# Kernel optimization log

Hardware: AMD Instinct MI355X
Metric: run time of the kernel (lower is better)

The kernel has to match this reference:

```python
import math
import jax, jax.numpy as jnp
import numpy as np

WS = 16        # window size (square)
SHIFT = 8      # window_size // 2 (window_shift=True)
NUM_HEADS = 6

def _rel_coords_table(ws):
    # Swin-V2 log-spaced continuous relative coords, shape (1, 2ws-1, 2ws-1, 2)
    r = np.arange(-(ws - 1), ws, dtype=np.float32)
    t = np.stack(np.meshgrid(r, r, indexing='ij'), axis=-1)[None]
    t = t / (ws - 1) * 8.0
    t = np.sign(t) * np.log2(np.abs(t) + 1.0) / np.log2(8.0)
    return t.astype(np.float32)

def _rel_pos_index(ws):
    ch, cw = np.meshgrid(np.arange(ws), np.arange(ws), indexing='ij')
    coords = np.stack([ch.ravel(), cw.ravel()])          # (2, N)
    rel = coords[:, :, None] - coords[:, None, :]        # (2, N, N)
    rel = rel.transpose(1, 2, 0).astype(np.int64)
    rel[..., 0] += ws - 1
    rel[..., 1] += ws - 1
    rel[..., 0] *= 2 * ws - 1
    return rel.sum(-1).astype(np.int32)                  # (N, N), values in [0, (2ws-1)^2)

def _shift_mask(H, W, ws, shift):
    img = np.zeros((H, W), dtype=np.float32)
    cnt = 0
    for hs in (slice(0, -ws), slice(-ws, -shift), slice(-shift, None)):
        for wsl in (slice(0, -ws), slice(-ws, -shift), slice(-shift, None)):
            img[hs, wsl] = cnt; cnt += 1
    win = img.reshape(H // ws, ws, W // ws, ws).transpose(0, 2, 1, 3).reshape(-1, ws * ws)
    diff = win[:, None, :] - win[:, :, None]
    return np.where(diff != 0, -100.0, 0.0).astype(np.float32)  # (nW, N, N)

def setup_inputs():
    key = jax.random.key(0)
    ks = jax.random.split(key, 4)
    B, H, W = 16, 64, 64
    C = 3 * NUM_HEADS * 32  # 576 (qkv channels)
    qkv = jax.random.normal(ks[0], (B, H * W, C), dtype=jnp.float32)
    table = jnp.asarray(_rel_coords_table(WS))
    index = jnp.asarray(_rel_pos_index(WS))
    mask = jnp.asarray(_shift_mask(H, W, WS, SHIFT))
    logit_scale = jnp.log(10.0 * jnp.ones((NUM_HEADS, 1, 1), dtype=jnp.float32))
    w1 = jax.random.normal(ks[1], (512, 2), dtype=jnp.float32) * 0.02
    b1 = jnp.zeros((512,), dtype=jnp.float32)
    w2 = jax.random.normal(ks[2], (NUM_HEADS, 512), dtype=jnp.float32) * 0.02
    return {"qkv": qkv, "table": table, "mask": mask, "logit_scale": logit_scale,
            "w1": w1, "b1": b1, "w2": w2, "index": index, "H": H, "W": W}

def reference(qkv, table, mask, logit_scale, w1, b1, w2, index, H, W):
    B, L, C = qkv.shape
    dim = C // 3
    hd = dim // NUM_HEADS
    x = qkv.reshape(B, H, W, C)
    x = jnp.roll(x, (-SHIFT, -SHIFT), axis=(1, 2))
    nWh, nWw = H // WS, W // WS
    # window partition -> (B_, N, C)
    x = x.reshape(B, nWh, WS, nWw, WS, C).transpose(0, 1, 3, 2, 4, 5).reshape(-1, WS * WS, C)
    B_, N, _ = x.shape
    qkv_ = x.reshape(B_, N, 3, NUM_HEADS, hd).transpose(2, 0, 3, 1, 4)
    q, k, v = qkv_[0], qkv_[1], qkv_[2]  # (B_, H, N, hd)
    # cosine attention
    qn = q / jnp.maximum(jnp.linalg.norm(q, axis=-1, keepdims=True), 1e-12)
    kn = k / jnp.maximum(jnp.linalg.norm(k, axis=-1, keepdims=True), 1e-12)
    attn = jnp.einsum('bhnd,bhmd->bhnm', qn, kn)
    scale = jnp.exp(jnp.minimum(logit_scale, math.log(1.0 / 0.01)))  # (H,1,1)
    attn = attn * scale[None]
    # CPB MLP bias: Linear(2,512)+ReLU -> Linear(512,H,no bias)
    hidden = jax.nn.relu(table @ w1.T + b1)          # (1, 2ws-1, 2ws-1, 512)
    bias_table = (hidden @ w2.T).reshape(-1, NUM_HEADS)
    bias = bias_table[index.reshape(-1)].reshape(N, N, NUM_HEADS).transpose(2, 0, 1)
    attn = attn + 16.0 * jax.nn.sigmoid(bias)[None]
    # shifted-window mask
    nWm = mask.shape[0]
    attn = attn.reshape(B_ // nWm, nWm, NUM_HEADS, N, N) + mask[None, :, None]
    attn = attn.reshape(B_, NUM_HEADS, N, N)
    attn = jax.nn.softmax(attn, axis=-1)
    out = jnp.einsum('bhnm,bhmd->bhnd', attn, v)
    out = out.transpose(0, 2, 1, 3).reshape(B_, N, dim)
    # window reverse + unshift
    out = out.reshape(B, nWh, nWw, WS, WS, dim).transpose(0, 1, 3, 2, 4, 5).reshape(B, H, W, dim)
    out = jnp.roll(out, (SHIFT, SHIFT), axis=(1, 2))
    return out.reshape(B, L, dim)
```

## Files before the change

kernel.cpp:

```cpp
#include <hip/hip_runtime.h>
#include <cstdint>

#define NH 6
#define HD 32
#define NTOK 256
#define CIN 576
#define DIMO 192
#define LOG2E 1.44269504f
#define SHIFT2 37.6f
#define MNEG (-144.269504f)

typedef short short8 __attribute__((ext_vector_type(8)));
typedef float f32x4 __attribute__((ext_vector_type(4)));

__device__ __forceinline__ int grp6(int x) { return (x < 48) ? 0 : ((x < 56) ? 1 : 2); }

__device__ __forceinline__ unsigned short f2bf(float f) {
    unsigned int u = __float_as_uint(f);
    u += 0x7fffu + ((u >> 16) & 1u);
    return (unsigned short)(u >> 16);
}
__device__ __forceinline__ float bf2f(unsigned short s) {
    return __uint_as_float(((unsigned)s) << 16);
}

__global__ void cpb_kernel(const float* __restrict__ table,
                           const float* __restrict__ w1,
                           const float* __restrict__ b1,
                           const float* __restrict__ w2,
                           float* __restrict__ bv) {
    __shared__ float hid[512];
    int p = blockIdx.x;
    float t0 = table[2 * p], t1 = table[2 * p + 1];
    int t = threadIdx.x;
    for (int j = t; j < 512; j += 256) {
        float hv = fmaf(t0, w1[2 * j], fmaf(t1, w1[2 * j + 1], b1[j]));
        hid[j] = fmaxf(hv, 0.f);
    }
    __syncthreads();
    if (t < 192) {
        int h = t >> 5, l = t & 31;
        const float* w2h = w2 + h * 512;
        float acc = 0.f;
        for (int j = l; j < 512; j += 32) acc = fmaf(hid[j], w2h[j], acc);
        acc += __shfl_xor(acc, 1, 32);
        acc += __shfl_xor(acc, 2, 32);
        acc += __shfl_xor(acc, 4, 32);
        acc += __shfl_xor(acc, 8, 32);
        acc += __shfl_xor(acc, 16, 32);
        if (l == 0) bv[h * 961 + p] = (16.f / (1.f + __expf(-acc))) * LOG2E;
    }
}

__global__ __launch_bounds__(512, 4) void attn_kernel(
    const float* __restrict__ qkv,
    const float* __restrict__ logit_scale,
    const float* __restrict__ bv,
    float* __restrict__ out)
{
    __shared__ __align__(16) short Qb[NTOK * HD];
    __shared__ __align__(16) short Kb[NTOK * HD];
    __shared__ __align__(16) short Vt[HD * 264];
    __shared__ __align__(16) short P[8 * 32 * 32];
    __shared__ float Bv[961];

    const int t = threadIdx.x;
    const int h = blockIdx.x % NH;
    const int win = blockIdx.x / NH;
    const int b = win >> 4, wl = win & 15, wh = wl >> 2, ww = wl & 3;

    const float scale2 = __expf(fminf(logit_scale[h], 4.6051702f)) * LOG2E;

    for (int p = t; p < 961; p += 512) Bv[p] = bv[h * 961 + p];

    {
        int n = (t < 256) ? t : (t - 256);
        int i = n >> 4, j = n & 15;
        int rr = wh * 16 + i, cc = ww * 16 + j;
        int r = (rr + 8) & 63, c = (cc + 8) & 63;
        const float* base = qkv + ((long)(b * 4096 + r * 64 + c)) * CIN + h * HD;
        if (t < 256) {
            float qv[32], kv[32];
            const float4* qp = (const float4*)base;
            const float4* kp = (const float4*)(base + DIMO);
#pragma unroll
            for (int w = 0; w < 8; ++w) {
                float4 x = qp[w];
                qv[4 * w + 0] = x.x; qv[4 * w + 1] = x.y; qv[4 * w + 2] = x.z; qv[4 * w + 3] = x.w;
            }
#pragma unroll
            for (int w = 0; w < 8; ++w) {
                float4 x = kp[w];
                kv[4 * w + 0] = x.x; kv[4 * w + 1] = x.y; kv[4 * w + 2] = x.z; kv[4 * w + 3] = x.w;
            }
            float sq = 0.f, sk = 0.f;
#pragma unroll
            for (int d = 0; d < 32; ++d) { sq = fmaf(qv[d], qv[d], sq); sk = fmaf(kv[d], kv[d], sk); }
            float qs = scale2 / fmaxf(sqrtf(sq), 1e-12f);
            float ks = 1.f / fmaxf(sqrtf(sk), 1e-12f);
#pragma unroll
            for (int w = 0; w < 4; ++w) {
                short8 qc, kc;
#pragma unroll
                for (int e = 0; e < 8; ++e) {
                    qc[e] = (short)f2bf(qv[8 * w + e] * qs);
                    kc[e] = (short)f2bf(kv[8 * w + e] * ks);
                }
                *(short8*)&Qb[n * 32 + 8 * w] = qc;
                *(short8*)&Kb[n * 32 + 8 * w] = kc;
            }
        } else {
            float vv[32];
            const float4* vp = (const float4*)(base + 2 * DIMO);
#pragma unroll
            for (int w = 0; w < 8; ++w) {
                float4 x = vp[w];
                vv[4 * w + 0] = x.x; vv[4 * w + 1] = x.y; vv[4 * w + 2] = x.z; vv[4 * w + 3] = x.w;
            }
#pragma unroll
            for (int d = 0; d < 32; ++d) Vt[d * 264 + n] = (short)f2bf(vv[d]);
        }
    }
    __syncthreads();

    const int wv = t >> 6, lane = t & 63, quad = lane >> 4, l15 = lane & 15;
    short* Pw = P + wv * 1024;

    int trg[2];
    short8 aQ[2];
#pragma unroll
    for (int tl = 0; tl < 2; ++tl) {
        trg[tl] = wv * 2 + tl;
        aQ[tl] = *(const short8*)&Qb[(trg[tl] * 16 + l15) * 32 + quad * 8];
    }
    int gqi[2];
#pragma unroll
    for (int tl = 0; tl < 2; ++tl) gqi[tl] = grp6(wh * 16 + trg[tl]);
    int gqj[4];
#pragma unroll
    for (int reg = 0; reg < 4; ++reg) gqj[reg] = grp6(ww * 16 + quad * 4 + reg);
    const int gmj = grp6(ww * 16 + l15);

    f32x4 O[2][2];
    float lp[2][4];
#pragma unroll
    for (int tl = 0; tl < 2; ++tl)
#pragma unroll
        for (int dtk = 0; dtk < 2; ++dtk) O[tl][dtk] = (f32x4){0.f, 0.f, 0.f, 0.f};
#pragma unroll
    for (int tl = 0; tl < 2; ++tl)
#pragma unroll
        for (int reg = 0; reg < 4; ++reg) lp[tl][reg] = 0.f;

    const f32x4 Zero = (f32x4){0.f, 0.f, 0.f, 0.f};

    for (int c = 0; c < 8; ++c) {
        short8 bK[2];
        int gmi[2], ctg[2];
#pragma unroll
        for (int ct = 0; ct < 2; ++ct) {
            ctg[ct] = c * 2 + ct;
            bK[ct] = *(const short8*)&Kb[(ctg[ct] * 16 + l15) * 32 + quad * 8];
            gmi[ct] = grp6(wh * 16 + ctg[ct]);
        }
        f32x4 S[2][2];
#pragma unroll
        for (int tl = 0; tl < 2; ++tl)
#pragma unroll
            for (int ct = 0; ct < 2; ++ct)
                S[tl][ct] = __builtin_amdgcn_mfma_f32_16x16x32_bf16(aQ[tl], bK[ct], Zero, 0, 0, 0);

#pragma unroll
        for (int tl = 0; tl < 2; ++tl) {
#pragma unroll
            for (int ct = 0; ct < 2; ++ct) {
                int rbase = (trg[tl] - ctg[ct] + 15) * 31 + 15 - l15;
                bool mi = (gqi[tl] == gmi[ct]);
#pragma unroll
                for (int reg = 0; reg < 4; ++reg) {
                    float bias = Bv[rbase + quad * 4 + reg];
                    float mterm = (mi && (gqj[reg] == gmj)) ? 0.f : MNEG;
                    float arg = S[tl][ct][reg] + bias + mterm - SHIFT2;
                    float e = __builtin_amdgcn_exp2f(arg);
                    unsigned short pb = f2bf(e);
                    lp[tl][reg] += bf2f(pb);
                    Pw[(tl * 16 + quad * 4 + reg) * 32 + ct * 16 + l15] = (short)pb;
                }
            }
        }

        short8 aP[2], bV[2];
#pragma unroll
        for (int tl = 0; tl < 2; ++tl)
            aP[tl] = *(const short8*)&Pw[(tl * 16 + l15) * 32 + quad * 8];
#pragma unroll
        for (int dtk = 0; dtk < 2; ++dtk)
            bV[dtk] = *(const short8*)&Vt[(dtk * 16 + l15) * 264 + c * 32 + quad * 8];
#pragma unroll
        for (int tl = 0; tl < 2; ++tl)
#pragma unroll
            for (int dtk = 0; dtk < 2; ++dtk)
                O[tl][dtk] = __builtin_amdgcn_mfma_f32_16x16x32_bf16(aP[tl], bV[dtk], O[tl][dtk], 0, 0, 0);
    }

#pragma unroll
    for (int tl = 0; tl < 2; ++tl)
#pragma unroll
        for (int reg = 0; reg < 4; ++reg) {
            float s = lp[tl][reg];
            s += __shfl_xor(s, 1, 16);
            s += __shfl_xor(s, 2, 16);
            s += __shfl_xor(s, 4, 16);
            s += __shfl_xor(s, 8, 16);
            lp[tl][reg] = 1.f / s;
        }

    const long pixb = (long)b * 4096;
#pragma unroll
    for (int tl = 0; tl < 2; ++tl) {
        int r = (wh * 16 + trg[tl] + 8) & 63;
#pragma unroll
        for (int reg = 0; reg < 4; ++reg) {
            int cpix = (ww * 16 + quad * 4 + reg + 8) & 63;
            float* op = out + (pixb + r * 64 + cpix) * DIMO + h * HD + l15;
            float inv = lp[tl][reg];
            op[0]  = O[tl][0][reg] * inv;
            op[16] = O[tl][1][reg] * inv;
        }
    }
}

extern "C" void kernel_launch(void* const* d_in, const int* in_sizes, int n_in,
                              void* d_out, int out_size, void* d_ws, size_t ws_size,
                              hipStream_t stream) {
    const float* qkv         = (const float*)d_in[0];
    const float* table       = (const float*)d_in[1];
    const float* logit_scale = (const float*)d_in[3];
    const float* w1          = (const float*)d_in[4];
    const float* b1          = (const float*)d_in[5];
    const float* w2          = (const float*)d_in[6];
    float* out = (float*)d_out;
    float* bv  = (float*)d_ws;

    cpb_kernel<<<961, 256, 0, stream>>>(table, w1, b1, w2, bv);
    attn_kernel<<<256 * NH, 512, 0, stream>>>(qkv, logit_scale, bv, out);
}
```

Baseline: 264.7 us.

## Keep softmax probabilities in registers via transposed S and permlane swap

Computes S transposed (K as the A operand, Q as the B operand) so that each lane holds probabilities for one query. The probabilities are then packed to bf16 with v_cvt_pk_bf16_f32 and rearranged with v_permlane32_swap into the MFMA A-operand layout, removing the per-wave P shared-memory round trip. The change also XOR-swizzles the Q/K LDS layout to cut bank conflicts, and permutes and pairs the V-transpose stores as 32-bit writes. It folds the SHIFT2 constant into the bias table and sums probabilities in fp32 instead of their rounded bf16 values, which slightly changes the softmax normalization numerics.

```diff
diff --git a/kernel.cpp b/kernel.cpp
--- a/kernel.cpp
+++ b/kernel.cpp
@@ -12,6 +12,7 @@
 
 typedef short short8 __attribute__((ext_vector_type(8)));
 typedef float f32x4 __attribute__((ext_vector_type(4)));
+typedef int   int4v __attribute__((ext_vector_type(4)));
 
 __device__ __forceinline__ int grp6(int x) { return (x < 48) ? 0 : ((x < 56) ? 1 : 2); }
 
@@ -20,8 +21,9 @@
     u += 0x7fffu + ((u >> 16) & 1u);
     return (unsigned short)(u >> 16);
 }
-__device__ __forceinline__ float bf2f(unsigned short s) {
-    return __uint_as_float(((unsigned)s) << 16);
+
+__device__ __forceinline__ int qk_off(int tile, int row, int quad) {
+    return tile * 512 + row * 32 + ((quad ^ ((row >> 1) & 3)) << 3);
 }
 
 __global__ void cpb_kernel(const float* __restrict__ table,
@@ -48,7 +50,7 @@
         acc += __shfl_xor(acc, 4, 32);
         acc += __shfl_xor(acc, 8, 32);
         acc += __shfl_xor(acc, 16, 32);
-        if (l == 0) bv[h * 961 + p] = (16.f / (1.f + __expf(-acc))) * LOG2E;
+        if (l == 0) bv[h * 961 + p] = (16.f / (1.f + __expf(-acc))) * LOG2E - SHIFT2;
     }
 }
 
@@ -61,7 +63,6 @@
     __shared__ __align__(16) short Qb[NTOK * HD];
     __shared__ __align__(16) short Kb[NTOK * HD];
     __shared__ __align__(16) short Vt[HD * 264];
-    __shared__ __align__(16) short P[8 * 32 * 32];
     __shared__ float Bv[961];
 
     const int t = threadIdx.x;
@@ -74,12 +75,12 @@
     for (int p = t; p < 961; p += 512) Bv[p] = bv[h * 961 + p];
 
     {
-        int n = (t < 256) ? t : (t - 256);
-        int i = n >> 4, j = n & 15;
-        int rr = wh * 16 + i, cc = ww * 16 + j;
-        int r = (rr + 8) & 63, c = (cc + 8) & 63;
-        const float* base = qkv + ((long)(b * 4096 + r * 64 + c)) * CIN + h * HD;
         if (t < 256) {
+            int n = t;
+            int i = n >> 4, j = n & 15;
+            int rr = wh * 16 + i, cc = ww * 16 + j;
+            int r = (rr + 8) & 63, c0 = (cc + 8) & 63;
+            const float* base = qkv + ((long)(b * 4096 + r * 64 + c0)) * CIN + h * HD;
             float qv[32], kv[32];
             const float4* qp = (const float4*)base;
             const float4* kp = (const float4*)(base + DIMO);
@@ -106,126 +107,133 @@
                     qc[e] = (short)f2bf(qv[8 * w + e] * qs);
                     kc[e] = (short)f2bf(kv[8 * w + e] * ks);
                 }
-                *(short8*)&Qb[n * 32 + 8 * w] = qc;
-                *(short8*)&Kb[n * 32 + 8 * w] = kc;
+                int off = qk_off(i, j, w);
+                *(short8*)&Qb[off] = qc;
+                *(short8*)&Kb[off] = kc;
             }
         } else {
-            float vv[32];
-            const float4* vp = (const float4*)(base + 2 * DIMO);
-#pragma unroll
-            for (int w = 0; w < 8; ++w) {
-                float4 x = vp[w];
-                vv[4 * w + 0] = x.x; vv[4 * w + 1] = x.y; vv[4 * w + 2] = x.z; vv[4 * w + 3] = x.w;
-            }
-#pragma unroll
-            for (int d = 0; d < 32; ++d) Vt[d * 264 + n] = (short)f2bf(vv[d]);
+            int n2 = t - 256;
+            int m = n2 & 127, dh = n2 >> 7;
+            int i = m >> 3;
+            int ja = (2 * m) & 15;
+            int r  = (wh * 16 + i + 8) & 63;
+            int ca = (ww * 16 + ja + 8) & 63;
+            int cb = (ww * 16 + ja + 1 + 8) & 63;
+            const float* ba = qkv + ((long)(b * 4096 + r * 64 + ca)) * CIN + h * HD + 2 * DIMO + dh * 16;
+            const float* bb = qkv + ((long)(b * 4096 + r * 64 + cb)) * CIN + h * HD + 2 * DIMO + dh * 16;
+            float va[16], vb[16];
+            const float4* pa4 = (const float4*)ba;
+            const float4* pb4 = (const float4*)bb;
+#pragma unroll
+            for (int w = 0; w < 4; ++w) {
+                float4 A = pa4[w], B = pb4[w];
+                va[4 * w + 0] = A.x; va[4 * w + 1] = A.y; va[4 * w + 2] = A.z; va[4 * w + 3] = A.w;
+                vb[4 * w + 0] = B.x; vb[4 * w + 1] = B.y; vb[4 * w + 2] = B.z; vb[4 * w + 3] = B.w;
+            }
+            int u = m & 15;
+            int jp = ((u & 1) << 3) | ((u & 2) << 1) | ((u & 4) >> 1) | ((u & 8) >> 3);
+            int colb = (m >> 4) * 32 + 2 * jp;
+#pragma unroll
+            for (int di = 0; di < 16; ++di) {
+                unsigned pa_ = f2bf(va[di]);
+                unsigned pb_ = f2bf(vb[di]);
+                *(unsigned*)&Vt[(dh * 16 + di) * 264 + colb] = pa_ | (pb_ << 16);
+            }
         }
     }
     __syncthreads();
 
     const int wv = t >> 6, lane = t & 63, quad = lane >> 4, l15 = lane & 15;
-    short* Pw = P + wv * 1024;
-
-    int trg[2];
-    short8 aQ[2];
-#pragma unroll
-    for (int tl = 0; tl < 2; ++tl) {
-        trg[tl] = wv * 2 + tl;
-        aQ[tl] = *(const short8*)&Qb[(trg[tl] * 16 + l15) * 32 + quad * 8];
-    }
-    int gqi[2];
-#pragma unroll
-    for (int tl = 0; tl < 2; ++tl) gqi[tl] = grp6(wh * 16 + trg[tl]);
-    int gqj[4];
-#pragma unroll
-    for (int reg = 0; reg < 4; ++reg) gqj[reg] = grp6(ww * 16 + quad * 4 + reg);
-    const int gmj = grp6(ww * 16 + l15);
+
+    int trg[2] = {wv * 2, wv * 2 + 1};
+    short8 bQ[2];
+#pragma unroll
+    for (int tl = 0; tl < 2; ++tl)
+        bQ[tl] = *(const short8*)&Qb[qk_off(trg[tl], l15, quad)];
+
+    int gqr[2];
+#pragma unroll
+    for (int tl = 0; tl < 2; ++tl) gqr[tl] = grp6(wh * 16 + trg[tl]);
+    const int gcl = grp6(ww * 16 + l15);
+    float cm[4];
+#pragma unroll
+    for (int reg = 0; reg < 4; ++reg)
+        cm[reg] = (gcl == grp6(ww * 16 + quad * 4 + reg)) ? 0.f : MNEG;
 
     f32x4 O[2][2];
-    float lp[2][4];
+    float lp[2] = {0.f, 0.f};
 #pragma unroll
     for (int tl = 0; tl < 2; ++tl)
 #pragma unroll
         for (int dtk = 0; dtk < 2; ++dtk) O[tl][dtk] = (f32x4){0.f, 0.f, 0.f, 0.f};
-#pragma unroll
-    for (int tl = 0; tl < 2; ++tl)
-#pragma unroll
-        for (int reg = 0; reg < 4; ++reg) lp[tl][reg] = 0.f;
 
     const f32x4 Zero = (f32x4){0.f, 0.f, 0.f, 0.f};
 
     for (int c = 0; c < 8; ++c) {
-        short8 bK[2];
-        int gmi[2], ctg[2];
-#pragma unroll
-        for (int ct = 0; ct < 2; ++ct) {
-            ctg[ct] = c * 2 + ct;
-            bK[ct] = *(const short8*)&Kb[(ctg[ct] * 16 + l15) * 32 + quad * 8];
-            gmi[ct] = grp6(wh * 16 + ctg[ct]);
-        }
-        f32x4 S[2][2];
-#pragma unroll
-        for (int tl = 0; tl < 2; ++tl)
-#pragma unroll
-            for (int ct = 0; ct < 2; ++ct)
-                S[tl][ct] = __builtin_amdgcn_mfma_f32_16x16x32_bf16(aQ[tl], bK[ct], Zero, 0, 0, 0);
-
-#pragma unroll
-        for (int tl = 0; tl < 2; ++tl) {
-#pragma unroll
-            for (int ct = 0; ct < 2; ++ct) {
-                int rbase = (trg[tl] - ctg[ct] + 15) * 31 + 15 - l15;
-                bool mi = (gqi[tl] == gmi[ct]);
-#pragma unroll
-                for (int reg = 0; reg < 4; ++reg) {
-                    float bias = Bv[rbase + quad * 4 + reg];
-                    float mterm = (mi && (gqj[reg] == gmj)) ? 0.f : MNEG;
-                    float arg = S[tl][ct][reg] + bias + mterm - SHIFT2;
-                    float e = __builtin_amdgcn_exp2f(arg);
-                    unsigned short pb = f2bf(e);
-                    lp[tl][reg] += bf2f(pb);
-                    Pw[(tl * 16 + quad * 4 + reg) * 32 + ct * 16 + l15] = (short)pb;
-                }
-            }
-        }
-
-        short8 aP[2], bV[2];
-#pragma unroll
-        for (int tl = 0; tl < 2; ++tl)
-            aP[tl] = *(const short8*)&Pw[(tl * 16 + l15) * 32 + quad * 8];
+        int ctg[2] = {2 * c, 2 * c + 1};
+        short8 aK[2], bV[2];
+#pragma unroll
+        for (int ct = 0; ct < 2; ++ct)
+            aK[ct] = *(const short8*)&Kb[qk_off(ctg[ct], l15, quad)];
 #pragma unroll
         for (int dtk = 0; dtk < 2; ++dtk)
             bV[dtk] = *(const short8*)&Vt[(dtk * 16 + l15) * 264 + c * 32 + quad * 8];
+
+        f32x4 S[2][2];
 #pragma unroll
         for (int tl = 0; tl < 2; ++tl)
 #pragma unroll
-            for (int dtk = 0; dtk < 2; ++dtk)
-                O[tl][dtk] = __builtin_amdgcn_mfma_f32_16x16x32_bf16(aP[tl], bV[dtk], O[tl][dtk], 0, 0, 0);
-    }
-
-#pragma unroll
-    for (int tl = 0; tl < 2; ++tl)
+            for (int ct = 0; ct < 2; ++ct)
+                S[tl][ct] = __builtin_amdgcn_mfma_f32_16x16x32_bf16(aK[ct], bQ[tl], Zero, 0, 0, 0);
+
+        int gkr[2] = {grp6(wh * 16 + ctg[0]), grp6(wh * 16 + ctg[1])};
+
+#pragma unroll
+        for (int tl = 0; tl < 2; ++tl) {
+            float ev[2][4];
+#pragma unroll
+            for (int ct = 0; ct < 2; ++ct) {
+                int rb = (trg[tl] - ctg[ct] + 15) * 31 + 15 + l15 - 4 * quad;
+                bool rmatch = (gqr[tl] == gkr[ct]);
+#pragma unroll
+                for (int reg = 0; reg < 4; ++reg) {
+                    float madd = rmatch ? cm[reg] : MNEG;
+                    float arg = S[tl][ct][reg] + (Bv[rb - reg] + madd);
+                    float e = __builtin_amdgcn_exp2f(arg);
+                    ev[ct][reg] = e;
+                    lp[tl] += e;
+                }
+            }
+            int p0, p1, p2, p3;
+            asm("v_cvt_pk_bf16_f32 %0, %1, %2" : "=v"(p0) : "v"(ev[0][0]), "v"(ev[0][1]));
+            asm("v_cvt_pk_bf16_f32 %0, %1, %2" : "=v"(p1) : "v"(ev[1][0]), "v"(ev[1][1]));
+            asm("v_cvt_pk_bf16_f32 %0, %1, %2" : "=v"(p2) : "v"(ev[0][2]), "v"(ev[0][3]));
+            asm("v_cvt_pk_bf16_f32 %0, %1, %2" : "=v"(p3) : "v"(ev[1][2]), "v"(ev[1][3]));
+            asm("v_permlane32_swap_b32 %0, %1" : "+v"(p0), "+v"(p2));
+            asm("v_permlane32_swap_b32 %0, %1" : "+v"(p1), "+v"(p3));
+            int4v w = {p0, p1, p2, p3};
+            union { int4v i; short8 s; } cvt; cvt.i = w;
+            short8 aP = cvt.s;
+            O[tl][0] = __builtin_amdgcn_mfma_f32_16x16x32_bf16(aP, bV[0], O[tl][0], 0, 0, 0);
+            O[tl][1] = __builtin_amdgcn_mfma_f32_16x16x32_bf16(aP, bV[1], O[tl][1], 0, 0, 0);
+        }
+    }
+
+    const long pixb = (long)b * 4096;
+#pragma unroll
+    for (int tl = 0; tl < 2; ++tl) {
+        float s = lp[tl];
+        s += __shfl_xor(s, 16);
+        s += __shfl_xor(s, 32);
+        float invf = 1.f / s;
+        int r = (wh * 16 + trg[tl] + 8) & 63;
 #pragma unroll
         for (int reg = 0; reg < 4; ++reg) {
-            float s = lp[tl][reg];
-            s += __shfl_xor(s, 1, 16);
-            s += __shfl_xor(s, 2, 16);
-            s += __shfl_xor(s, 4, 16);
-            s += __shfl_xor(s, 8, 16);
-            lp[tl][reg] = 1.f / s;
-        }
-
-    const long pixb = (long)b * 4096;
-#pragma unroll
-    for (int tl = 0; tl < 2; ++tl) {
-        int r = (wh * 16 + trg[tl] + 8) & 63;
-#pragma unroll
-        for (int reg = 0; reg < 4; ++reg) {
+            float iv = __shfl(invf, quad * 4 + reg);
             int cpix = (ww * 16 + quad * 4 + reg + 8) & 63;
             float* op = out + (pixb + r * 64 + cpix) * DIMO + h * HD + l15;
-            float inv = lp[tl][reg];
-            op[0]  = O[tl][0][reg] * inv;
-            op[16] = O[tl][1][reg] * inv;
+            op[0]  = O[tl][0][reg] * iv;
+            op[16] = O[tl][1][reg] * iv;
         }
     }
 }
```

After: 261.4 us. About the same (-1.2%).
